# Optimization experiments

Measured on AMD Instinct MI355X. Metric: run time of the kernel, lower is better.

## Reference

```python
import jax, jax.numpy as jnp
import numpy as np

B, S, IN, H, T, OUT = 128, 336, 64, 1024, 96, 1


def _lstm_step(h, c, x, W_ih, W_hh, b_ih, b_hh):
    # PyTorch LSTM cell: gates in (i, f, g, o) order
    g = x @ W_ih.T + b_ih + h @ W_hh.T + b_hh  # [B, 4H]
    i, f, gg, o = jnp.split(g, 4, axis=-1)
    c_new = jax.nn.sigmoid(f) * c + jax.nn.sigmoid(i) * jnp.tanh(gg)
    h_new = jax.nn.sigmoid(o) * jnp.tanh(c_new)
    return h_new, c_new


def setup_inputs() -> dict:
    key = jax.random.key(0)
    ks = jax.random.split(key, 12)
    s = 0.05
    return {
        "src": jax.random.normal(ks[0], (B, S, IN), jnp.float32),
        "enc_W_ih": jax.random.normal(ks[1], (4 * H, IN), jnp.float32) * s,
        "enc_W_hh": jax.random.normal(ks[2], (4 * H, H), jnp.float32) * s,
        "enc_b_ih": jax.random.normal(ks[3], (4 * H,), jnp.float32) * s,
        "enc_b_hh": jax.random.normal(ks[4], (4 * H,), jnp.float32) * s,
        "dec_W_ih": jax.random.normal(ks[5], (4 * H, OUT + H), jnp.float32) * s,
        "dec_W_hh": jax.random.normal(ks[6], (4 * H, H), jnp.float32) * s,
        "dec_b_ih": jax.random.normal(ks[7], (4 * H,), jnp.float32) * s,
        "dec_b_hh": jax.random.normal(ks[8], (4 * H,), jnp.float32) * s,
        "attn_W": jax.random.normal(ks[9], (H, H), jnp.float32) * s,
        "fc_W": jax.random.normal(ks[10], (OUT, H), jnp.float32) * s,
        "fc_b": jax.random.normal(ks[11], (OUT,), jnp.float32) * s,
        "target_len": T,
    }


def reference(src, enc_W_ih, enc_W_hh, enc_b_ih, enc_b_hh,
              dec_W_ih, dec_W_hh, dec_b_ih, dec_b_hh,
              attn_W, fc_W, fc_b, target_len):
    batch = src.shape[0]
    hdim = enc_W_hh.shape[1]

    # ---- Encoder: single-layer LSTM over src, batch_first ----
    def enc_step(carry, x_t):
        h, c = carry
        h, c = _lstm_step(h, c, x_t, enc_W_ih, enc_W_hh, enc_b_ih, enc_b_hh)
        return (h, c), h

    h0 = jnp.zeros((batch, hdim), src.dtype)
    c0 = jnp.zeros((batch, hdim), src.dtype)
    (h_enc, c_enc), enc_hs = jax.lax.scan(enc_step, (h0, c0),
                                          jnp.swapaxes(src, 0, 1))
    encoder_outputs = jnp.swapaxes(enc_hs, 0, 1)  # [B, S, H]

    def dec_step(carry, _):
        h, c, prev_y = carry
        q = h @ attn_W.T                                      # [B, H]
        energy = jnp.einsum('bh,bsh->bs', q, encoder_outputs)  # [B, S]
        w = jax.nn.softmax(energy, axis=-1)
        ctx = jnp.einsum('bs,bsh->bh', w, encoder_outputs)     # [B, H]
        x = jnp.concatenate([prev_y, ctx], axis=-1)            # [B, OUT+H]
        h, c = _lstm_step(h, c, x, dec_W_ih, dec_W_hh, dec_b_ih, dec_b_hh)
        pred = h @ fc_W.T + fc_b                               # [B, OUT]
        prev_y = jax.lax.stop_gradient(pred)                   # pred.detach()
        return (h, c, prev_y), pred

    prev_y0 = jnp.zeros((batch, fc_W.shape[0]), src.dtype)
    _, preds = jax.lax.scan(dec_step, (h_enc, c_enc, prev_y0), None,
                            length=target_len)
    return jnp.swapaxes(preds, 0, 1)  # [B, target_len, OUT]
```

## Files before the change

### kernel.cpp

```cpp
#include <hip/hip_runtime.h>
#include <math.h>

#define Bn   128
#define Sn   336
#define INd  64
#define Hn   1024
#define Tn   96
#define G4   4096
#define KCE  34
#define KCD  65
#define KCQ  32
#define NBLK 256

typedef __attribute__((ext_vector_type(8))) short short8;
typedef __attribute__((ext_vector_type(4))) float floatx4;
typedef __attribute__((ext_vector_type(4))) unsigned int uintx4;
typedef unsigned long long u64t;

__device__ __forceinline__ float sigmoidf_(float x){ return 1.0f/(1.0f+expf(-x)); }

__device__ __forceinline__ unsigned short f2bf(float f){
    union { float f; unsigned u; } v; v.f = f;
    unsigned r = v.u + 0x7fffu + ((v.u >> 16) & 1u);
    return (unsigned short)(r >> 16);
}
__device__ __forceinline__ float bflo(unsigned u){ union{unsigned u; float f;} v; v.u = u << 16;        return v.f; }
__device__ __forceinline__ float bfhi(unsigned u){ union{unsigned u; float f;} v; v.u = u & 0xffff0000u; return v.f; }
__device__ __forceinline__ void unpack8v(uintx4 v, float* f){
    f[0]=bflo(v.x); f[1]=bfhi(v.x); f[2]=bflo(v.y); f[3]=bfhi(v.y);
    f[4]=bflo(v.z); f[5]=bfhi(v.z); f[6]=bflo(v.w); f[7]=bfhi(v.w);
}

union Frag16 { u64t q[2]; short8 s8; uintx4 u4; };

__device__ __forceinline__ short8 ld_cg_s8(const unsigned short* p){
    Frag16 r;
    r.q[0] = __hip_atomic_load((const u64t*)p,     __ATOMIC_RELAXED, __HIP_MEMORY_SCOPE_AGENT);
    r.q[1] = __hip_atomic_load((const u64t*)p + 1, __ATOMIC_RELAXED, __HIP_MEMORY_SCOPE_AGENT);
    return r.s8;
}
__device__ __forceinline__ uintx4 ld_cg_u4(const unsigned short* p){
    Frag16 r;
    r.q[0] = __hip_atomic_load((const u64t*)p,     __ATOMIC_RELAXED, __HIP_MEMORY_SCOPE_AGENT);
    r.q[1] = __hip_atomic_load((const u64t*)p + 1, __ATOMIC_RELAXED, __HIP_MEMORY_SCOPE_AGENT);
    return r.u4;
}
__device__ __forceinline__ void st_cg16(unsigned short* p, unsigned short v){
    asm volatile("global_store_short %0, %1, off sc0 sc1" :: "v"(p), "v"((unsigned)v) : "memory");
}
__device__ __forceinline__ void st_cg32(unsigned short* p, unsigned v){
    asm volatile("global_store_dword %0, %1, off sc0 sc1" :: "v"(p), "v"(v) : "memory");
}

__device__ __forceinline__ void gbar(unsigned* ctr, unsigned tgt){
    asm volatile("s_waitcnt vmcnt(0)" ::: "memory");
    __syncthreads();
    if (threadIdx.x == 0){
        __hip_atomic_fetch_add(ctr, 1u, __ATOMIC_RELAXED, __HIP_MEMORY_SCOPE_AGENT);
        while (__hip_atomic_load(ctr, __ATOMIC_RELAXED, __HIP_MEMORY_SCOPE_AGENT) < tgt)
            __builtin_amdgcn_s_sleep(2);
    }
    __syncthreads();
}

__global__ void pack_encf(const float* __restrict__ Wih, const float* __restrict__ Whh,
                          const float* __restrict__ bih, const float* __restrict__ bhh,
                          unsigned short* __restrict__ Wp, float* __restrict__ bc){
    long n = (long)256*KCE*512;
    for (long idx = (long)blockIdx.x*256 + threadIdx.x; idx < n; idx += (long)gridDim.x*256){
        int j = (int)(idx & 7), l = (int)((idx >> 3) & 63);
        int kc = (int)((idx >> 9) % KCE);
        int s  = (int)(idx / (KCE*512));
        int c = l & 15, kg = l >> 4;
        int k = kc*32 + kg*8 + j;
        int gate = s & 3, unit = (s >> 2)*16 + c;
        int orig = gate*Hn + unit;
        float v = (k < INd) ? Wih[orig*INd + k] : Whh[(size_t)orig*Hn + (k - INd)];
        Wp[idx] = f2bf(v);
    }
    int tid = blockIdx.x*256 + threadIdx.x;
    if (tid < G4){
        int g = (tid >> 4) & 3, u = (tid >> 6)*16 + (tid & 15);
        int orig = g*Hn + u;
        bc[tid] = bih[orig] + bhh[orig];
    }
}

__global__ void pack_decf(const float* __restrict__ Wih, const float* __restrict__ Whh,
                          const float* __restrict__ bih, const float* __restrict__ bhh,
                          unsigned short* __restrict__ Wp, float* __restrict__ bc){
    long n = (long)256*KCD*512;
    for (long idx = (long)blockIdx.x*256 + threadIdx.x; idx < n; idx += (long)gridDim.x*256){
        int j = (int)(idx & 7), l = (int)((idx >> 3) & 63);
        int kc = (int)((idx >> 9) % KCD);
        int s  = (int)(idx / (KCD*512));
        int c = l & 15, kg = l >> 4;
        int k = kc*32 + kg*8 + j;
        int gate = s & 3, unit = (s >> 2)*16 + c;
        int orig = gate*Hn + unit;
        float v;
        if (k < Hn)          v = Wih[(size_t)orig*(Hn+1) + 1 + k];
        else if (k < 2*Hn)   v = Whh[(size_t)orig*Hn + (k - Hn)];
        else if (k == 2*Hn)  v = Wih[(size_t)orig*(Hn+1)];
        else                 v = 0.0f;
        Wp[idx] = f2bf(v);
    }
    int tid = blockIdx.x*256 + threadIdx.x;
    if (tid < G4){
        int g = (tid >> 4) & 3, u = (tid >> 6)*16 + (tid & 15);
        int orig = g*Hn + u;
        bc[tid] = bih[orig] + bhh[orig];
    }
}

__global__ void pack_attnf(const float* __restrict__ w, unsigned short* __restrict__ Wp){
    int n = 64*KCQ*512;
    for (int idx = blockIdx.x*256 + threadIdx.x; idx < n; idx += gridDim.x*256){
        int j = idx & 7, l = (idx >> 3) & 63;
        int kc = (idx >> 9) & 31;
        int s  = idx >> 14;
        int nn = s*16 + (l & 15);
        int k = kc*32 + (l >> 4)*8 + j;
        Wp[idx] = f2bf(w[(size_t)nn*Hn + k]);
    }
}

__global__ void conv_srcf(const float* __restrict__ s, unsigned short* __restrict__ d){
    int n = Sn*8*2*512;
    for (int idx = blockIdx.x*256 + threadIdx.x; idx < n; idx += gridDim.x*256){
        int j = idx & 7, l = (idx >> 3) & 63;
        int kc = (idx >> 9) & 1, rg = (idx >> 10) & 7, t = idx >> 13;
        int b = rg*16 + (l & 15);
        int k = kc*32 + (l >> 4)*8 + j;
        d[idx] = f2bf(s[((size_t)b*Sn + t)*INd + k]);
    }
}

__global__ void init_ws(unsigned short* __restrict__ hf0, float* __restrict__ cbuf,
                        unsigned short* __restrict__ A0, unsigned short* __restrict__ A1,
                        unsigned* __restrict__ bars){
    int t0 = blockIdx.x*256 + threadIdx.x;
    if (t0 < 4) bars[t0] = 0;
    for (int i = t0; i < 8*KCD*512; i += gridDim.x*256){
        A0[i] = 0; A1[i] = 0;
        if (i < 8*32*512) hf0[i] = 0;
        if (i < Bn*Hn) cbuf[i] = 0.0f;
    }
}

__device__ __forceinline__ void swz(int b, int& x, int& y){
    int xcd = b & 7, li = b >> 3;
    y = xcd*8 + (li & 7);
    x = li >> 3;
}

__device__ __forceinline__ float fcdot(const unsigned short* __restrict__ hplain,
                                       const float* __restrict__ fcW, int b, int l){
    const unsigned short* hp = hplain + (size_t)b*Hn + l*16;
    uintx4 h0 = ld_cg_u4(hp), h1 = ld_cg_u4(hp + 8);
    float hf[16]; unpack8v(h0, hf); unpack8v(h1, hf + 8);
    float p = 0.0f;
    #pragma unroll
    for (int i = 0; i < 16; i++) p = fmaf(hf[i], fcW[l*16 + i], p);
    #pragma unroll
    for (int off = 32; off; off >>= 1) p += __shfl_down(p, off);
    return p;
}

__global__ __launch_bounds__(256, 1)
void enc_loop(const unsigned short* __restrict__ srcfrag,
              const unsigned short* __restrict__ Wf,
              const float* __restrict__ bc, float* __restrict__ cbuf,
              unsigned short* __restrict__ hf0,
              unsigned short* __restrict__ hf1,
              unsigned short* __restrict__ enco,
              unsigned short* __restrict__ adec0,
              unsigned* __restrict__ bar)
{
    __shared__ float red[2][16][65];
    const int tid = threadIdx.x, l = tid & 63, w = tid >> 6;
    const int rgw = w & 1, kh = w >> 1;
    int x, y; swz(blockIdx.x, x, y);
    const int rg = x*2 + rgw;
    const int m0 = rg*16;
    const unsigned short* Bf = Wf + (size_t)(4*y)*KCE*512 + l*8;

    const int col = l & 15, q = l >> 4;
    const int u = y*16 + col;
    const float bi  = bc[y*64 + col];
    const float bf_ = bc[y*64 + 16 + col];
    const float bg  = bc[y*64 + 32 + col];
    const float bo  = bc[y*64 + 48 + col];
    const int lsh = ((u >> 3) & 3) * 16;

    unsigned tgt = NBLK;
    for (int t = 0; t < Sn; t++){
        const unsigned short* hin = (t & 1) ? hf1 : hf0;
        unsigned short* hout      = (t & 1) ? hf0 : hf1;
        const unsigned short* Ah = hin + (size_t)rg*32*512 + l*8;
        floatx4 acc0={0,0,0,0}, acc1={0,0,0,0}, acc2={0,0,0,0}, acc3={0,0,0,0};

        if (kh == 0){
            const unsigned short* Ax = srcfrag + ((size_t)t*8 + rg)*2*512 + l*8;
            #pragma unroll
            for (int kc = 0; kc < 2; kc++){
                short8 a  = *(const short8*)(Ax + kc*512);
                short8 b0 = *(const short8*)(Bf + (0*KCE + kc)*512);
                short8 b1 = *(const short8*)(Bf + (1*KCE + kc)*512);
                short8 b2 = *(const short8*)(Bf + (2*KCE + kc)*512);
                short8 b3 = *(const short8*)(Bf + (3*KCE + kc)*512);
                acc0 = __builtin_amdgcn_mfma_f32_16x16x32_bf16(a, b0, acc0, 0, 0, 0);
                acc1 = __builtin_amdgcn_mfma_f32_16x16x32_bf16(a, b1, acc1, 0, 0, 0);
                acc2 = __builtin_amdgcn_mfma_f32_16x16x32_bf16(a, b2, acc2, 0, 0, 0);
                acc3 = __builtin_amdgcn_mfma_f32_16x16x32_bf16(a, b3, acc3, 0, 0, 0);
            }
            #pragma unroll 5
            for (int hc = 0; hc < 15; hc++){
                short8 a  = ld_cg_s8(Ah + hc*512);
                short8 b0 = *(const short8*)(Bf + (0*KCE + hc + 2)*512);
                short8 b1 = *(const short8*)(Bf + (1*KCE + hc + 2)*512);
                short8 b2 = *(const short8*)(Bf + (2*KCE + hc + 2)*512);
                short8 b3 = *(const short8*)(Bf + (3*KCE + hc + 2)*512);
                acc0 = __builtin_amdgcn_mfma_f32_16x16x32_bf16(a, b0, acc0, 0, 0, 0);
                acc1 = __builtin_amdgcn_mfma_f32_16x16x32_bf16(a, b1, acc1, 0, 0, 0);
                acc2 = __builtin_amdgcn_mfma_f32_16x16x32_bf16(a, b2, acc2, 0, 0, 0);
                acc3 = __builtin_amdgcn_mfma_f32_16x16x32_bf16(a, b3, acc3, 0, 0, 0);
            }
        } else {
            #pragma unroll 5
            for (int hc = 15; hc < 32; hc++){
                short8 a  = ld_cg_s8(Ah + hc*512);
                short8 b0 = *(const short8*)(Bf + (0*KCE + hc + 2)*512);
                short8 b1 = *(const short8*)(Bf + (1*KCE + hc + 2)*512);
                short8 b2 = *(const short8*)(Bf + (2*KCE + hc + 2)*512);
                short8 b3 = *(const short8*)(Bf + (3*KCE + hc + 2)*512);
                acc0 = __builtin_amdgcn_mfma_f32_16x16x32_bf16(a, b0, acc0, 0, 0, 0);
                acc1 = __builtin_amdgcn_mfma_f32_16x16x32_bf16(a, b1, acc1, 0, 0, 0);
                acc2 = __builtin_amdgcn_mfma_f32_16x16x32_bf16(a, b2, acc2, 0, 0, 0);
                acc3 = __builtin_amdgcn_mfma_f32_16x16x32_bf16(a, b3, acc3, 0, 0, 0);
            }
            #pragma unroll
            for (int r = 0; r < 4; r++){
                red[rgw][ 0 + r][l] = acc0[r];
                red[rgw][ 4 + r][l] = acc1[r];
                red[rgw][ 8 + r][l] = acc2[r];
                red[rgw][12 + r][l] = acc3[r];
            }
        }
        __syncthreads();
        if (kh == 0){
            #pragma unroll
            for (int r = 0; r < 4; r++){
                acc0[r] += red[rgw][ 0 + r][l];
                acc1[r] += red[rgw][ 4 + r][l];
                acc2[r] += red[rgw][ 8 + r][l];
                acc3[r] += red[rgw][12 + r][l];
            }
            #pragma unroll
            for (int r = 0; r < 4; r++){
                const int m = m0 + q*4 + r;
                float gi = acc0[r] + bi;
                float gf = acc1[r] + bf_;
                float gg = acc2[r] + bg;
                float go = acc3[r] + bo;
                float co = cbuf[(size_t)m*Hn + u];
                float cn = sigmoidf_(gf)*co + sigmoidf_(gi)*tanhf(gg);
                float hv = sigmoidf_(go)*tanhf(cn);
                cbuf[(size_t)m*Hn + u] = cn;
                unsigned short hb = f2bf(hv);
                const int lanep = (q*4 + r) + lsh;
                st_cg16(hout + (((size_t)rg*32 + (u >> 5))*64 + lanep)*8 + (u & 7), hb);
                enco[((size_t)m*Sn + t)*Hn + u] = hb;
                if (t == Sn-1) adec0[(((size_t)rg*KCD + 32 + (u >> 5))*64 + lanep)*8 + (u & 7)] = hb;
            }
        }
        gbar(bar, tgt); tgt += NBLK;
    }
}

__global__ __launch_bounds__(512, 1)
void dec_loop(unsigned short* __restrict__ A0, unsigned short* __restrict__ A1,
              const unsigned short* __restrict__ Wdec,
              const float* __restrict__ bdec, float* __restrict__ cbuf,
              const unsigned short* __restrict__ Watt,
              unsigned short* __restrict__ qbf,
              const unsigned short* __restrict__ enco,
              unsigned short* __restrict__ hplain,
              const float* __restrict__ fcW, const float* __restrict__ fcb,
              float* __restrict__ out, unsigned* __restrict__ bar)
{
    __shared__ float smem[8224];
    const int tid = threadIdx.x, l = tid & 63, w = tid >> 6;
    const int rgw = w & 1, ks = w >> 1;
    int x, y; swz(blockIdx.x, x, y);
    const int rg = x*2 + rgw, m0 = rg*16;
    const unsigned short* Bf = Wdec + (size_t)(4*y)*KCD*512 + l*8;

    const int col = l & 15, q4 = l >> 4;
    const int u = y*16 + col;
    const float bi  = bdec[y*64 + col];
    const float bf_ = bdec[y*64 + 16 + col];
    const float bg  = bdec[y*64 + 32 + col];
    const float bo  = bdec[y*64 + 48 + col];
    const int lsh = ((u >> 3) & 3) * 16;
    const int ka0 = (ks==0) ? 32 : (ks==1) ? 42 : (ks==2) ? 46 : 55;
    const int ka1 = (ks==0) ? 42 : (ks==1) ? 46 : (ks==2) ? 55 : 64;

    unsigned tgt = NBLK;
    for (int d = 0; d < Tn; d++){
        unsigned short* Ac = (d & 1) ? A1 : A0;
        unsigned short* An = (d & 1) ? A0 : A1;
        const unsigned short* Af = Ac + (size_t)rg*KCD*512 + l*8;

        floatx4 acc0={0,0,0,0}, acc1={0,0,0,0}, acc2={0,0,0,0}, acc3={0,0,0,0};
        #pragma unroll 2
        for (int kc = ka0; kc < ka1; kc++){
            short8 a  = ld_cg_s8(Af + kc*512);
            short8 b0 = *(const short8*)(Bf + (0*KCD + kc)*512);
            short8 b1 = *(const short8*)(Bf + (1*KCD + kc)*512);
            short8 b2 = *(const short8*)(Bf + (2*KCD + kc)*512);
            short8 b3 = *(const short8*)(Bf + (3*KCD + kc)*512);
            acc0 = __builtin_amdgcn_mfma_f32_16x16x32_bf16(a, b0, acc0, 0, 0, 0);
            acc1 = __builtin_amdgcn_mfma_f32_16x16x32_bf16(a, b1, acc1, 0, 0, 0);
            acc2 = __builtin_amdgcn_mfma_f32_16x16x32_bf16(a, b2, acc2, 0, 0, 0);
            acc3 = __builtin_amdgcn_mfma_f32_16x16x32_bf16(a, b3, acc3, 0, 0, 0);
        }
        if (ks == 1){
            const unsigned short* Aq = Ac + ((size_t)rg*KCD + 32)*512 + l*8;
            const unsigned short* Bq = Watt + (size_t)y*KCQ*512 + l*8;
            floatx4 qa = {0,0,0,0};
            #pragma unroll 4
            for (int kc = 0; kc < KCQ; kc++){
                short8 a = ld_cg_s8(Aq + kc*512);
                short8 b = *(const short8*)(Bq + kc*512);
                qa = __builtin_amdgcn_mfma_f32_16x16x32_bf16(a, b, qa, 0, 0, 0);
            }
            #pragma unroll
            for (int r = 0; r < 4; r++)
                st_cg16(qbf + (size_t)(m0 + q4*4 + r)*Hn + y*16 + col, f2bf(qa[r]));
        }
        if (d > 0 && x == 0 && w >= 6){
            const int b = y*2 + (w & 1);
            float p = fcdot(hplain, fcW, b, l);
            if (l == 0){
                float pv = p + fcb[0];
                out[b*Tn + (d-1)] = pv;
                st_cg16(Ac + (((size_t)(b >> 4))*KCD + 64)*512 + (b & 15)*8, f2bf(pv));
            }
        }
        gbar(bar, tgt); tgt += NBLK;

        if (blockIdx.x < Bn){
            const int b = blockIdx.x;
            float* ctxl = smem;
            float* mred = smem + 8192;
            float* lred = smem + 8200;
            float qv[16];
            {
                const unsigned short* qp = qbf + (size_t)b*Hn + l*16;
                uintx4 q0 = ld_cg_u4(qp), q1 = ld_cg_u4(qp + 8);
                unpack8v(q0, qv); unpack8v(q1, qv + 8);
            }
            float mx = -1e30f, lsum = 0.0f;
            float cacc[16];
            #pragma unroll
            for (int i = 0; i < 16; i++) cacc[i] = 0.0f;

            const uintx4* ebase = (const uintx4*)(enco + (size_t)b*Sn*Hn) + l*2;
            for (int s = w; s < Sn; s += 8){
                uintx4 e0 = ebase[(size_t)s*128];
                uintx4 e1 = ebase[(size_t)s*128 + 1];
                float ev[16];
                unpack8v(e0, ev); unpack8v(e1, ev + 8);
                float part = 0.0f;
                #pragma unroll
                for (int i = 0; i < 16; i++) part = fmaf(qv[i], ev[i], part);
                #pragma unroll
                for (int off = 32; off; off >>= 1) part += __shfl_down(part, off);
                float e = __shfl(part, 0);
                float mn = fmaxf(mx, e);
                float corr = expf(mx - mn);
                float p = expf(e - mn);
                lsum = lsum*corr + p;
                if (corr != 1.0f){
                    #pragma unroll
                    for (int i = 0; i < 16; i++) cacc[i] *= corr;
                }
                #pragma unroll
                for (int i = 0; i < 16; i++) cacc[i] = fmaf(p, ev[i], cacc[i]);
                mx = mn;
            }
            if (l == 0){ mred[w] = mx; lred[w] = lsum; }
            __syncthreads();
            float M = mred[0];
            #pragma unroll
            for (int k = 1; k < 8; k++) M = fmaxf(M, mred[k]);
            float corr2 = expf(mx - M);
            #pragma unroll
            for (int j = 0; j < 16; j++) ctxl[w*1024 + j*64 + l] = cacc[j]*corr2;
            __syncthreads();
            float L = 0.0f;
            #pragma unroll
            for (int k = 0; k < 8; k++) L += lred[k]*expf(mred[k] - M);
            float invL = 1.0f / L;

            const int u0 = 2*tid;
            float s0 = 0.0f, s1 = 0.0f;
            #pragma unroll
            for (int k = 0; k < 8; k++){
                s0 += ctxl[k*1024 + (u0 & 15)*64 + (u0 >> 4)];
                s1 += ctxl[k*1024 + ((u0+1) & 15)*64 + ((u0+1) >> 4)];
            }
            unsigned cvu = (unsigned)f2bf(s0*invL) | ((unsigned)f2bf(s1*invL) << 16);
            const int kcw = u0 >> 5;
            const int lanep2 = (b & 15) + ((u0 >> 3) & 3)*16;
            st_cg32(Ac + ((((size_t)(b >> 4))*KCD + kcw)*64 + lanep2)*8 + (u0 & 7), cvu);
        }
        gbar(bar, tgt); tgt += NBLK;

        {
            const int kc0 = ks*8;
            #pragma unroll 2
            for (int kk = 0; kk < 8; kk++){
                const int kc = kc0 + kk;
                short8 a  = ld_cg_s8(Af + kc*512);
                short8 b0 = *(const short8*)(Bf + (0*KCD + kc)*512);
                short8 b1 = *(const short8*)(Bf + (1*KCD + kc)*512);
                short8 b2 = *(const short8*)(Bf + (2*KCD + kc)*512);
                short8 b3 = *(const short8*)(Bf + (3*KCD + kc)*512);
                acc0 = __builtin_amdgcn_mfma_f32_16x16x32_bf16(a, b0, acc0, 0, 0, 0);
                acc1 = __builtin_amdgcn_mfma_f32_16x16x32_bf16(a, b1, acc1, 0, 0, 0);
                acc2 = __builtin_amdgcn_mfma_f32_16x16x32_bf16(a, b2, acc2, 0, 0, 0);
                acc3 = __builtin_amdgcn_mfma_f32_16x16x32_bf16(a, b3, acc3, 0, 0, 0);
            }
            if (ks == 3){
                short8 a  = ld_cg_s8(Af + 64*512);
                short8 b0 = *(const short8*)(Bf + (0*KCD + 64)*512);
                short8 b1 = *(const short8*)(Bf + (1*KCD + 64)*512);
                short8 b2 = *(const short8*)(Bf + (2*KCD + 64)*512);
                short8 b3 = *(const short8*)(Bf + (3*KCD + 64)*512);
                acc0 = __builtin_amdgcn_mfma_f32_16x16x32_bf16(a, b0, acc0, 0, 0, 0);
                acc1 = __builtin_amdgcn_mfma_f32_16x16x32_bf16(a, b1, acc1, 0, 0, 0);
                acc2 = __builtin_amdgcn_mfma_f32_16x16x32_bf16(a, b2, acc2, 0, 0, 0);
                acc3 = __builtin_amdgcn_mfma_f32_16x16x32_bf16(a, b3, acc3, 0, 0, 0);
            }
        }
        if (ks != 0){
            float* rp = smem + ((ks-1)*2 + rgw)*1024;
            #pragma unroll
            for (int r = 0; r < 4; r++){
                rp[( 0 + r)*64 + l] = acc0[r];
                rp[( 4 + r)*64 + l] = acc1[r];
                rp[( 8 + r)*64 + l] = acc2[r];
                rp[(12 + r)*64 + l] = acc3[r];
            }
        }
        __syncthreads();
        if (ks == 0){
            const float* r0 = smem + rgw*1024;
            const float* r1 = smem + (2 + rgw)*1024;
            const float* r2 = smem + (4 + rgw)*1024;
            #pragma unroll
            for (int r = 0; r < 4; r++){
                acc0[r] += r0[( 0+r)*64 + l] + r1[( 0+r)*64 + l] + r2[( 0+r)*64 + l];
                acc1[r] += r0[( 4+r)*64 + l] + r1[( 4+r)*64 + l] + r2[( 4+r)*64 + l];
                acc2[r] += r0[( 8+r)*64 + l] + r1[( 8+r)*64 + l] + r2[( 8+r)*64 + l];
                acc3[r] += r0[(12+r)*64 + l] + r1[(12+r)*64 + l] + r2[(12+r)*64 + l];
            }
            #pragma unroll
            for (int r = 0; r < 4; r++){
                const int m = m0 + q4*4 + r;
                float gi = acc0[r] + bi;
                float gf = acc1[r] + bf_;
                float gg = acc2[r] + bg;
                float go = acc3[r] + bo;
                float co = cbuf[(size_t)m*Hn + u];
                float cn = sigmoidf_(gf)*co + sigmoidf_(gi)*tanhf(gg);
                float hv = sigmoidf_(go)*tanhf(cn);
                cbuf[(size_t)m*Hn + u] = cn;
                unsigned short hb = f2bf(hv);
                const int lanep = (q4*4 + r) + lsh;
                st_cg16(An + (((size_t)rg*KCD + 32 + (u >> 5))*64 + lanep)*8 + (u & 7), hb);
                st_cg16(hplain + (size_t)m*Hn + u, hb);
            }
        }
        gbar(bar, tgt); tgt += NBLK;
    }

    if (x == 0 && w >= 6){
        const int b = y*2 + (w & 1);
        float p = fcdot(hplain, fcW, b, l);
        if (l == 0) out[b*Tn + (Tn - 1)] = p + fcb[0];
    }
}

extern "C" void kernel_launch(void* const* d_in, const int* in_sizes, int n_in,
                              void* d_out, int out_size, void* d_ws, size_t ws_size,
                              hipStream_t stream){
    const float* src  = (const float*)d_in[0];
    const float* eWih = (const float*)d_in[1];
    const float* eWhh = (const float*)d_in[2];
    const float* ebih = (const float*)d_in[3];
    const float* ebhh = (const float*)d_in[4];
    const float* dWih = (const float*)d_in[5];
    const float* dWhh = (const float*)d_in[6];
    const float* dbih = (const float*)d_in[7];
    const float* dbhh = (const float*)d_in[8];
    const float* attnW= (const float*)d_in[9];
    const float* fcW  = (const float*)d_in[10];
    const float* fcb  = (const float*)d_in[11];
    float* out = (float*)d_out;

    char* base = (char*)d_ws;
    auto alloc = [&](size_t bytes){ void* p = base; base += (bytes + 255) & ~255ull; return p; };
    unsigned short* Wencf = (unsigned short*)alloc((size_t)256*KCE*512*2);
    float*          benc  = (float*)alloc(G4*4);
    unsigned short* Wdecf = (unsigned short*)alloc((size_t)256*KCD*512*2);
    float*          bdec  = (float*)alloc(G4*4);
    unsigned short* Wattf = (unsigned short*)alloc((size_t)64*KCQ*512*2);
    unsigned short* srcf  = (unsigned short*)alloc((size_t)Sn*8*2*512*2);
    unsigned short* enco  = (unsigned short*)alloc((size_t)Bn*Sn*Hn*2);
    unsigned short* hf0   = (unsigned short*)alloc((size_t)8*32*512*2);
    unsigned short* hf1   = (unsigned short*)alloc((size_t)8*32*512*2);
    float*          cbuf  = (float*)alloc((size_t)Bn*Hn*4);
    unsigned short* A0f   = (unsigned short*)alloc((size_t)8*KCD*512*2);
    unsigned short* A1f   = (unsigned short*)alloc((size_t)8*KCD*512*2);
    unsigned short* qbf   = (unsigned short*)alloc((size_t)Bn*Hn*2);
    unsigned short* hplain= (unsigned short*)alloc((size_t)Bn*Hn*2);
    unsigned*       bars  = (unsigned*)alloc(4*4);

    conv_srcf<<<2048, 256, 0, stream>>>(src, srcf);
    pack_encf<<<4096, 256, 0, stream>>>(eWih, eWhh, ebih, ebhh, Wencf, benc);
    pack_decf<<<8192, 256, 0, stream>>>(dWih, dWhh, dbih, dbhh, Wdecf, bdec);
    pack_attnf<<<1024, 256, 0, stream>>>(attnW, Wattf);
    init_ws<<<1040, 256, 0, stream>>>(hf0, cbuf, A0f, A1f, bars);

    enc_loop<<<NBLK, 256, 0, stream>>>(srcf, Wencf, benc, cbuf, hf0, hf1,
                                       enco, A0f, bars + 0);
    dec_loop<<<NBLK, 512, 0, stream>>>(A0f, A1f, Wdecf, bdec, cbuf, Wattf,
                                       qbf, enco, hplain, fcW, fcb, out, bars + 1);
}
```

Baseline: 10.17 ms.

## Use hierarchical grid barrier, split attention across all blocks, batch fragment loads

Replaces the single-counter grid barrier with a two-level barrier. Blocks are grouped by XCD, one representative per group gathers the group and then releases it through a per-group flag. This cuts contention on one atomic. The decoder attention now runs on all 256 blocks, each covering half the source sequence. The partial max/sum/context values are merged in an extra barrier phase. The attention query projection is spread across all four k-slices instead of one warp. Hidden-state fragments are prefetched into registers before the MFMA loops. The trade-off is an extra grid barrier per decoder step and higher register pressure.

```diff
diff --git a/kernel.cpp b/kernel.cpp
--- a/kernel.cpp
+++ b/kernel.cpp
@@ -11,6 +11,7 @@
 #define KCD  65
 #define KCQ  32
 #define NBLK 256
+#define SHALF 168
 
 typedef __attribute__((ext_vector_type(8))) short short8;
 typedef __attribute__((ext_vector_type(4))) float floatx4;
@@ -32,6 +33,7 @@
 }
 
 union Frag16 { u64t q[2]; short8 s8; uintx4 u4; };
+union F2 { u64t q; float f[2]; };
 
 __device__ __forceinline__ short8 ld_cg_s8(const unsigned short* p){
     Frag16 r;
@@ -51,14 +53,31 @@
 __device__ __forceinline__ void st_cg32(unsigned short* p, unsigned v){
     asm volatile("global_store_dword %0, %1, off sc0 sc1" :: "v"(p), "v"(v) : "memory");
 }
-
-__device__ __forceinline__ void gbar(unsigned* ctr, unsigned tgt){
+__device__ __forceinline__ void st_cg64(float* p, float a, float b){
+    F2 v; v.f[0] = a; v.f[1] = b;
+    __hip_atomic_store((u64t*)p, v.q, __ATOMIC_RELAXED, __HIP_MEMORY_SCOPE_AGENT);
+}
+__device__ __forceinline__ F2 ld_cg64(const float* p){
+    F2 v; v.q = __hip_atomic_load((const u64t*)p, __ATOMIC_RELAXED, __HIP_MEMORY_SCOPE_AGENT);
+    return v;
+}
+
+__device__ __forceinline__ void gbar2(unsigned* bb, int g, bool rep, unsigned step){
     asm volatile("s_waitcnt vmcnt(0)" ::: "memory");
     __syncthreads();
     if (threadIdx.x == 0){
-        __hip_atomic_fetch_add(ctr, 1u, __ATOMIC_RELAXED, __HIP_MEMORY_SCOPE_AGENT);
-        while (__hip_atomic_load(ctr, __ATOMIC_RELAXED, __HIP_MEMORY_SCOPE_AGENT) < tgt)
-            __builtin_amdgcn_s_sleep(2);
+        __hip_atomic_fetch_add(bb + g*32, 1u, __ATOMIC_RELAXED, __HIP_MEMORY_SCOPE_AGENT);
+        if (rep){
+            while (__hip_atomic_load(bb + g*32, __ATOMIC_RELAXED, __HIP_MEMORY_SCOPE_AGENT) < step*32u)
+                __builtin_amdgcn_s_sleep(1);
+            __hip_atomic_fetch_add(bb + 256, 1u, __ATOMIC_RELAXED, __HIP_MEMORY_SCOPE_AGENT);
+            while (__hip_atomic_load(bb + 256, __ATOMIC_RELAXED, __HIP_MEMORY_SCOPE_AGENT) < step*8u)
+                __builtin_amdgcn_s_sleep(1);
+            __hip_atomic_store(bb + 512 + g*32, step, __ATOMIC_RELAXED, __HIP_MEMORY_SCOPE_AGENT);
+        } else {
+            while (__hip_atomic_load(bb + 512 + g*32, __ATOMIC_RELAXED, __HIP_MEMORY_SCOPE_AGENT) < step)
+                __builtin_amdgcn_s_sleep(1);
+        }
     }
     __syncthreads();
 }
@@ -140,7 +159,7 @@
                         unsigned short* __restrict__ A0, unsigned short* __restrict__ A1,
                         unsigned* __restrict__ bars){
     int t0 = blockIdx.x*256 + threadIdx.x;
-    if (t0 < 4) bars[t0] = 0;
+    if (t0 < 2048) bars[t0] = 0;
     for (int i = t0; i < 8*KCD*512; i += gridDim.x*256){
         A0[i] = 0; A1[i] = 0;
         if (i < 8*32*512) hf0[i] = 0;
@@ -181,6 +200,8 @@
     const int tid = threadIdx.x, l = tid & 63, w = tid >> 6;
     const int rgw = w & 1, kh = w >> 1;
     int x, y; swz(blockIdx.x, x, y);
+    const int g = blockIdx.x & 7;
+    const bool rep = (blockIdx.x >> 3) == 0;
     const int rg = x*2 + rgw;
     const int m0 = rg*16;
     const unsigned short* Bf = Wf + (size_t)(4*y)*KCE*512 + l*8;
@@ -193,7 +214,7 @@
     const float bo  = bc[y*64 + 48 + col];
     const int lsh = ((u >> 3) & 3) * 16;
 
-    unsigned tgt = NBLK;
+    unsigned bstep = 0;
     for (int t = 0; t < Sn; t++){
         const unsigned short* hin = (t & 1) ? hf1 : hf0;
         unsigned short* hout      = (t & 1) ? hf0 : hf1;
@@ -201,6 +222,9 @@
         floatx4 acc0={0,0,0,0}, acc1={0,0,0,0}, acc2={0,0,0,0}, acc3={0,0,0,0};
 
         if (kh == 0){
+            short8 ah[15];
+            #pragma unroll
+            for (int hc = 0; hc < 15; hc++) ah[hc] = ld_cg_s8(Ah + hc*512);
             const unsigned short* Ax = srcfrag + ((size_t)t*8 + rg)*2*512 + l*8;
             #pragma unroll
             for (int kc = 0; kc < 2; kc++){
@@ -214,30 +238,31 @@
                 acc2 = __builtin_amdgcn_mfma_f32_16x16x32_bf16(a, b2, acc2, 0, 0, 0);
                 acc3 = __builtin_amdgcn_mfma_f32_16x16x32_bf16(a, b3, acc3, 0, 0, 0);
             }
-            #pragma unroll 5
+            #pragma unroll
             for (int hc = 0; hc < 15; hc++){
-                short8 a  = ld_cg_s8(Ah + hc*512);
                 short8 b0 = *(const short8*)(Bf + (0*KCE + hc + 2)*512);
                 short8 b1 = *(const short8*)(Bf + (1*KCE + hc + 2)*512);
                 short8 b2 = *(const short8*)(Bf + (2*KCE + hc + 2)*512);
                 short8 b3 = *(const short8*)(Bf + (3*KCE + hc + 2)*512);
-                acc0 = __builtin_amdgcn_mfma_f32_16x16x32_bf16(a, b0, acc0, 0, 0, 0);
-                acc1 = __builtin_amdgcn_mfma_f32_16x16x32_bf16(a, b1, acc1, 0, 0, 0);
-                acc2 = __builtin_amdgcn_mfma_f32_16x16x32_bf16(a, b2, acc2, 0, 0, 0);
-                acc3 = __builtin_amdgcn_mfma_f32_16x16x32_bf16(a, b3, acc3, 0, 0, 0);
+                acc0 = __builtin_amdgcn_mfma_f32_16x16x32_bf16(ah[hc], b0, acc0, 0, 0, 0);
+                acc1 = __builtin_amdgcn_mfma_f32_16x16x32_bf16(ah[hc], b1, acc1, 0, 0, 0);
+                acc2 = __builtin_amdgcn_mfma_f32_16x16x32_bf16(ah[hc], b2, acc2, 0, 0, 0);
+                acc3 = __builtin_amdgcn_mfma_f32_16x16x32_bf16(ah[hc], b3, acc3, 0, 0, 0);
             }
         } else {
-            #pragma unroll 5
-            for (int hc = 15; hc < 32; hc++){
-                short8 a  = ld_cg_s8(Ah + hc*512);
-                short8 b0 = *(const short8*)(Bf + (0*KCE + hc + 2)*512);
-                short8 b1 = *(const short8*)(Bf + (1*KCE + hc + 2)*512);
-                short8 b2 = *(const short8*)(Bf + (2*KCE + hc + 2)*512);
-                short8 b3 = *(const short8*)(Bf + (3*KCE + hc + 2)*512);
-                acc0 = __builtin_amdgcn_mfma_f32_16x16x32_bf16(a, b0, acc0, 0, 0, 0);
-                acc1 = __builtin_amdgcn_mfma_f32_16x16x32_bf16(a, b1, acc1, 0, 0, 0);
-                acc2 = __builtin_amdgcn_mfma_f32_16x16x32_bf16(a, b2, acc2, 0, 0, 0);
-                acc3 = __builtin_amdgcn_mfma_f32_16x16x32_bf16(a, b3, acc3, 0, 0, 0);
+            short8 ah[17];
+            #pragma unroll
+            for (int i = 0; i < 17; i++) ah[i] = ld_cg_s8(Ah + (15 + i)*512);
+            #pragma unroll
+            for (int i = 0; i < 17; i++){
+                short8 b0 = *(const short8*)(Bf + (0*KCE + i + 17)*512);
+                short8 b1 = *(const short8*)(Bf + (1*KCE + i + 17)*512);
+                short8 b2 = *(const short8*)(Bf + (2*KCE + i + 17)*512);
+                short8 b3 = *(const short8*)(Bf + (3*KCE + i + 17)*512);
+                acc0 = __builtin_amdgcn_mfma_f32_16x16x32_bf16(ah[i], b0, acc0, 0, 0, 0);
+                acc1 = __builtin_amdgcn_mfma_f32_16x16x32_bf16(ah[i], b1, acc1, 0, 0, 0);
+                acc2 = __builtin_amdgcn_mfma_f32_16x16x32_bf16(ah[i], b2, acc2, 0, 0, 0);
+                acc3 = __builtin_amdgcn_mfma_f32_16x16x32_bf16(ah[i], b3, acc3, 0, 0, 0);
             }
             #pragma unroll
             for (int r = 0; r < 4; r++){
@@ -274,7 +299,7 @@
                 if (t == Sn-1) adec0[(((size_t)rg*KCD + 32 + (u >> 5))*64 + lanep)*8 + (u & 7)] = hb;
             }
         }
-        gbar(bar, tgt); tgt += NBLK;
+        bstep++; gbar2(bar, g, rep, bstep);
     }
 }
 
@@ -286,6 +311,8 @@
               unsigned short* __restrict__ qbf,
               const unsigned short* __restrict__ enco,
               unsigned short* __restrict__ hplain,
+              float* __restrict__ pctx,
+              float* __restrict__ pml,
               const float* __restrict__ fcW, const float* __restrict__ fcb,
               float* __restrict__ out, unsigned* __restrict__ bar)
 {
@@ -293,8 +320,11 @@
     const int tid = threadIdx.x, l = tid & 63, w = tid >> 6;
     const int rgw = w & 1, ks = w >> 1;
     int x, y; swz(blockIdx.x, x, y);
+    const int g = blockIdx.x & 7;
+    const bool rep = (blockIdx.x >> 3) == 0;
     const int rg = x*2 + rgw, m0 = rg*16;
     const unsigned short* Bf = Wdec + (size_t)(4*y)*KCD*512 + l*8;
+    const unsigned short* Bq = Watt + (size_t)y*KCQ*512 + l*8;
 
     const int col = l & 15, q4 = l >> 4;
     const int u = y*16 + col;
@@ -303,41 +333,47 @@
     const float bg  = bdec[y*64 + 32 + col];
     const float bo  = bdec[y*64 + 48 + col];
     const int lsh = ((u >> 3) & 3) * 16;
-    const int ka0 = (ks==0) ? 32 : (ks==1) ? 42 : (ks==2) ? 46 : 55;
-    const int ka1 = (ks==0) ? 42 : (ks==1) ? 46 : (ks==2) ? 55 : 64;
-
-    unsigned tgt = NBLK;
+    const int ab   = blockIdx.x & 127;
+    const int part = blockIdx.x >> 7;
+
+    unsigned bstep = 0;
     for (int d = 0; d < Tn; d++){
         unsigned short* Ac = (d & 1) ? A1 : A0;
         unsigned short* An = (d & 1) ? A0 : A1;
         const unsigned short* Af = Ac + (size_t)rg*KCD*512 + l*8;
 
         floatx4 acc0={0,0,0,0}, acc1={0,0,0,0}, acc2={0,0,0,0}, acc3={0,0,0,0};
-        #pragma unroll 2
-        for (int kc = ka0; kc < ka1; kc++){
-            short8 a  = ld_cg_s8(Af + kc*512);
-            short8 b0 = *(const short8*)(Bf + (0*KCD + kc)*512);
-            short8 b1 = *(const short8*)(Bf + (1*KCD + kc)*512);
-            short8 b2 = *(const short8*)(Bf + (2*KCD + kc)*512);
-            short8 b3 = *(const short8*)(Bf + (3*KCD + kc)*512);
-            acc0 = __builtin_amdgcn_mfma_f32_16x16x32_bf16(a, b0, acc0, 0, 0, 0);
-            acc1 = __builtin_amdgcn_mfma_f32_16x16x32_bf16(a, b1, acc1, 0, 0, 0);
-            acc2 = __builtin_amdgcn_mfma_f32_16x16x32_bf16(a, b2, acc2, 0, 0, 0);
-            acc3 = __builtin_amdgcn_mfma_f32_16x16x32_bf16(a, b3, acc3, 0, 0, 0);
-        }
-        if (ks == 1){
-            const unsigned short* Aq = Ac + ((size_t)rg*KCD + 32)*512 + l*8;
-            const unsigned short* Bq = Watt + (size_t)y*KCQ*512 + l*8;
+        {
+            short8 aA[8];
+            #pragma unroll
+            for (int kk = 0; kk < 8; kk++)
+                aA[kk] = ld_cg_s8(Af + (32 + ks*8 + kk)*512);
             floatx4 qa = {0,0,0,0};
-            #pragma unroll 4
-            for (int kc = 0; kc < KCQ; kc++){
-                short8 a = ld_cg_s8(Aq + kc*512);
-                short8 b = *(const short8*)(Bq + kc*512);
-                qa = __builtin_amdgcn_mfma_f32_16x16x32_bf16(a, b, qa, 0, 0, 0);
-            }
-            #pragma unroll
-            for (int r = 0; r < 4; r++)
-                st_cg16(qbf + (size_t)(m0 + q4*4 + r)*Hn + y*16 + col, f2bf(qa[r]));
+            #pragma unroll
+            for (int kk = 0; kk < 8; kk++){
+                const int kc = 32 + ks*8 + kk;
+                short8 b0 = *(const short8*)(Bf + (0*KCD + kc)*512);
+                short8 b1 = *(const short8*)(Bf + (1*KCD + kc)*512);
+                short8 b2 = *(const short8*)(Bf + (2*KCD + kc)*512);
+                short8 b3 = *(const short8*)(Bf + (3*KCD + kc)*512);
+                short8 bq = *(const short8*)(Bq + (ks*8 + kk)*512);
+                acc0 = __builtin_amdgcn_mfma_f32_16x16x32_bf16(aA[kk], b0, acc0, 0, 0, 0);
+                acc1 = __builtin_amdgcn_mfma_f32_16x16x32_bf16(aA[kk], b1, acc1, 0, 0, 0);
+                acc2 = __builtin_amdgcn_mfma_f32_16x16x32_bf16(aA[kk], b2, acc2, 0, 0, 0);
+                acc3 = __builtin_amdgcn_mfma_f32_16x16x32_bf16(aA[kk], b3, acc3, 0, 0, 0);
+                qa   = __builtin_amdgcn_mfma_f32_16x16x32_bf16(aA[kk], bq, qa, 0, 0, 0);
+            }
+            #pragma unroll
+            for (int r = 0; r < 4; r++) smem[(w*4 + r)*64 + l] = qa[r];
+        }
+        __syncthreads();
+        if (ks == 0){
+            #pragma unroll
+            for (int r = 0; r < 4; r++){
+                float s = smem[((0*2+rgw)*4 + r)*64 + l] + smem[((1*2+rgw)*4 + r)*64 + l]
+                        + smem[((2*2+rgw)*4 + r)*64 + l] + smem[((3*2+rgw)*4 + r)*64 + l];
+                st_cg16(qbf + (size_t)(m0 + q4*4 + r)*Hn + y*16 + col, f2bf(s));
+            }
         }
         if (d > 0 && x == 0 && w >= 6){
             const int b = y*2 + (w & 1);
@@ -348,16 +384,15 @@
                 st_cg16(Ac + (((size_t)(b >> 4))*KCD + 64)*512 + (b & 15)*8, f2bf(pv));
             }
         }
-        gbar(bar, tgt); tgt += NBLK;
-
-        if (blockIdx.x < Bn){
-            const int b = blockIdx.x;
+        bstep++; gbar2(bar, g, rep, bstep);
+
+        {
             float* ctxl = smem;
             float* mred = smem + 8192;
             float* lred = smem + 8200;
             float qv[16];
             {
-                const unsigned short* qp = qbf + (size_t)b*Hn + l*16;
+                const unsigned short* qp = qbf + (size_t)ab*Hn + l*16;
                 uintx4 q0 = ld_cg_u4(qp), q1 = ld_cg_u4(qp + 8);
                 unpack8v(q0, qv); unpack8v(q1, qv + 8);
             }
@@ -366,18 +401,19 @@
             #pragma unroll
             for (int i = 0; i < 16; i++) cacc[i] = 0.0f;
 
-            const uintx4* ebase = (const uintx4*)(enco + (size_t)b*Sn*Hn) + l*2;
-            for (int s = w; s < Sn; s += 8){
+            const uintx4* ebase = (const uintx4*)(enco + (size_t)ab*Sn*Hn) + l*2;
+            const int s0i = part*SHALF;
+            for (int s = s0i + w; s < s0i + SHALF; s += 8){
                 uintx4 e0 = ebase[(size_t)s*128];
                 uintx4 e1 = ebase[(size_t)s*128 + 1];
                 float ev[16];
                 unpack8v(e0, ev); unpack8v(e1, ev + 8);
-                float part = 0.0f;
+                float pt = 0.0f;
                 #pragma unroll
-                for (int i = 0; i < 16; i++) part = fmaf(qv[i], ev[i], part);
+                for (int i = 0; i < 16; i++) pt = fmaf(qv[i], ev[i], pt);
                 #pragma unroll
-                for (int off = 32; off; off >>= 1) part += __shfl_down(part, off);
-                float e = __shfl(part, 0);
+                for (int off = 32; off; off >>= 1) pt += __shfl_down(pt, off);
+                float e = __shfl(pt, 0);
                 float mn = fmaxf(mx, e);
                 float corr = expf(mx - mn);
                 float p = expf(e - mn);
@@ -402,7 +438,6 @@
             float L = 0.0f;
             #pragma unroll
             for (int k = 0; k < 8; k++) L += lred[k]*expf(mred[k] - M);
-            float invL = 1.0f / L;
 
             const int u0 = 2*tid;
             float s0 = 0.0f, s1 = 0.0f;
@@ -411,27 +446,46 @@
                 s0 += ctxl[k*1024 + (u0 & 15)*64 + (u0 >> 4)];
                 s1 += ctxl[k*1024 + ((u0+1) & 15)*64 + ((u0+1) >> 4)];
             }
-            unsigned cvu = (unsigned)f2bf(s0*invL) | ((unsigned)f2bf(s1*invL) << 16);
+            st_cg64(pctx + ((size_t)part*128 + ab)*1024 + u0, s0, s1);
+            if (tid == 0) st_cg64(pml + ((size_t)part*128 + ab)*2, M, L);
+        }
+        bstep++; gbar2(bar, g, rep, bstep);
+
+        if (blockIdx.x < Bn){
+            const int b = blockIdx.x;
+            F2 ml0 = ld_cg64(pml + (size_t)b*2);
+            F2 ml1 = ld_cg64(pml + (size_t)(128 + b)*2);
+            float M = fmaxf(ml0.f[0], ml1.f[0]);
+            float w0 = expf(ml0.f[0] - M), w1 = expf(ml1.f[0] - M);
+            float invL = 1.0f / (ml0.f[1]*w0 + ml1.f[1]*w1);
+            const int u0 = 2*tid;
+            F2 c0 = ld_cg64(pctx + (size_t)b*1024 + u0);
+            F2 c1 = ld_cg64(pctx + ((size_t)128 + b)*1024 + u0);
+            float v0 = (c0.f[0]*w0 + c1.f[0]*w1)*invL;
+            float v1 = (c0.f[1]*w0 + c1.f[1]*w1)*invL;
+            unsigned cvu = (unsigned)f2bf(v0) | ((unsigned)f2bf(v1) << 16);
             const int kcw = u0 >> 5;
             const int lanep2 = (b & 15) + ((u0 >> 3) & 3)*16;
             st_cg32(Ac + ((((size_t)(b >> 4))*KCD + kcw)*64 + lanep2)*8 + (u0 & 7), cvu);
         }
-        gbar(bar, tgt); tgt += NBLK;
+        bstep++; gbar2(bar, g, rep, bstep);
 
         {
-            const int kc0 = ks*8;
-            #pragma unroll 2
+            short8 aC[8];
+            #pragma unroll
+            for (int kk = 0; kk < 8; kk++)
+                aC[kk] = ld_cg_s8(Af + (ks*8 + kk)*512);
+            #pragma unroll
             for (int kk = 0; kk < 8; kk++){
-                const int kc = kc0 + kk;
-                short8 a  = ld_cg_s8(Af + kc*512);
+                const int kc = ks*8 + kk;
                 short8 b0 = *(const short8*)(Bf + (0*KCD + kc)*512);
                 short8 b1 = *(const short8*)(Bf + (1*KCD + kc)*512);
                 short8 b2 = *(const short8*)(Bf + (2*KCD + kc)*512);
                 short8 b3 = *(const short8*)(Bf + (3*KCD + kc)*512);
-                acc0 = __builtin_amdgcn_mfma_f32_16x16x32_bf16(a, b0, acc0, 0, 0, 0);
-                acc1 = __builtin_amdgcn_mfma_f32_16x16x32_bf16(a, b1, acc1, 0, 0, 0);
-                acc2 = __builtin_amdgcn_mfma_f32_16x16x32_bf16(a, b2, acc2, 0, 0, 0);
-                acc3 = __builtin_amdgcn_mfma_f32_16x16x32_bf16(a, b3, acc3, 0, 0, 0);
+                acc0 = __builtin_amdgcn_mfma_f32_16x16x32_bf16(aC[kk], b0, acc0, 0, 0, 0);
+                acc1 = __builtin_amdgcn_mfma_f32_16x16x32_bf16(aC[kk], b1, acc1, 0, 0, 0);
+                acc2 = __builtin_amdgcn_mfma_f32_16x16x32_bf16(aC[kk], b2, acc2, 0, 0, 0);
+                acc3 = __builtin_amdgcn_mfma_f32_16x16x32_bf16(aC[kk], b3, acc3, 0, 0, 0);
             }
             if (ks == 3){
                 short8 a  = ld_cg_s8(Af + 64*512);
@@ -484,7 +538,7 @@
                 st_cg16(hplain + (size_t)m*Hn + u, hb);
             }
         }
-        gbar(bar, tgt); tgt += NBLK;
+        bstep++; gbar2(bar, g, rep, bstep);
     }
 
     if (x == 0 && w >= 6){
@@ -527,7 +581,9 @@
     unsigned short* A1f   = (unsigned short*)alloc((size_t)8*KCD*512*2);
     unsigned short* qbf   = (unsigned short*)alloc((size_t)Bn*Hn*2);
     unsigned short* hplain= (unsigned short*)alloc((size_t)Bn*Hn*2);
-    unsigned*       bars  = (unsigned*)alloc(4*4);
+    float*          pctx  = (float*)alloc((size_t)2*128*1024*4);
+    float*          pml   = (float*)alloc((size_t)2*128*2*4);
+    unsigned*       bars  = (unsigned*)alloc(2048*4);
 
     conv_srcf<<<2048, 256, 0, stream>>>(src, srcf);
     pack_encf<<<4096, 256, 0, stream>>>(eWih, eWhh, ebih, ebhh, Wencf, benc);
@@ -538,5 +594,6 @@
     enc_loop<<<NBLK, 256, 0, stream>>>(srcf, Wencf, benc, cbuf, hf0, hf1,
                                        enco, A0f, bars + 0);
     dec_loop<<<NBLK, 512, 0, stream>>>(A0f, A1f, Wdecf, bdec, cbuf, Wattf,
-                                       qbf, enco, hplain, fcW, fcb, out, bars + 1);
-}
+                                       qbf, enco, hplain, pctx, pml,
+                                       fcW, fcb, out, bars + 1024);
+}
```

Measured after the change: 9.691 ms. -4.7%, faster.
